# Optimization experiments

Hardware: AMD Instinct MI355X
Metric: run time of the kernel (lower is better)

## Reference

```python
import jax, jax.numpy as jnp
import numpy as np

B, T, C = 4, 2048, 1024
H = 16
D = C // H  # head_size = 64


def setup_inputs() -> dict:
    key = jax.random.key(0)
    k1, k2, k3 = jax.random.split(key, 3)
    x = jax.random.normal(k1, (B, T, C), dtype=jnp.float32)
    # weights stored pre-transposed relative to torch nn.Linear: y = x @ w
    w_attn = jax.random.normal(k2, (C, 3 * C), dtype=jnp.float32) * (1.0 / np.sqrt(C))
    w_proj = jax.random.normal(k3, (C, C), dtype=jnp.float32) * (1.0 / np.sqrt(C))
    return {"x": x, "w_attn": w_attn, "w_proj": w_proj}


def reference(x, w_attn, w_proj):
    # Dropout layers are identity in eval mode (reference baseline).
    Bx, Tx, Cx = x.shape
    qkv = x @ w_attn                                   # [B,T,3C]
    q, k, v = jnp.split(qkv, 3, axis=2)
    # [B,T,C] -> [B,H,T,D]
    def heads(t):
        return t.reshape(Bx, Tx, H, D).transpose(0, 2, 1, 3)
    q, k, v = heads(q), heads(k), heads(v)
    scale = 1.0 / np.sqrt(D).astype(np.float32)
    att = jnp.einsum('bhqd,bhkd->bhqk', q, k) * scale   # [B,H,T,T]
    causal = jnp.tril(jnp.ones((Tx, Tx), dtype=bool))
    att = jnp.where(causal[None, None], att, -jnp.inf)
    att = jax.nn.softmax(att, axis=-1)
    y = jnp.einsum('bhqk,bhkd->bhqd', att, v)           # [B,H,T,D]
    y = y.transpose(0, 2, 1, 3).reshape(Bx, Tx, Cx)     # [B,T,C]
    return y @ w_proj
```

## Files before the change

### kernel.cpp

```cpp
#include <hip/hip_runtime.h>

typedef unsigned short ushort;
typedef short short8 __attribute__((ext_vector_type(8)));
typedef short short4v __attribute__((ext_vector_type(4)));
typedef float f32x4 __attribute__((ext_vector_type(4)));
typedef __attribute__((address_space(3))) unsigned int lds_u32;
typedef __attribute__((address_space(1))) const unsigned int glb_u32;

#define DEVI static __device__ __forceinline__

DEVI ushort f2b(float f) {
  union { float f; unsigned u; } x; x.f = f;
  unsigned r = x.u + 0x7fffu + ((x.u >> 16) & 1u);
  return (ushort)(r >> 16);
}

DEVI void gload_lds16(const ushort* g, ushort* l) {
  __builtin_amdgcn_global_load_lds((glb_u32*)g, (lds_u32*)l, 16, 0, 0);
}

__global__ __launch_bounds__(256) void prep_kernel(
    const float* __restrict__ x, const float* __restrict__ wa,
    const float* __restrict__ wp, ushort* __restrict__ xb,
    ushort* __restrict__ watT, ushort* __restrict__ wpT) {
  __shared__ float tile[32][33];
  const int bid = blockIdx.x, tid = threadIdx.x;
  if (bid < 4096) {
    int i = bid * 256 + tid;
    const float4* p = (const float4*)x + 2 * (size_t)i;
    float4 a = p[0], b = p[1];
    ushort tmp[8] = { f2b(a.x), f2b(a.y), f2b(a.z), f2b(a.w),
                      f2b(b.x), f2b(b.y), f2b(b.z), f2b(b.w) };
    *(short8*)(xb + 8 * (size_t)i) = *(short8*)tmp;
    return;
  }
  const float* in; ushort* out; int R, C, bx, by;
  if (bid < 7168) {
    int bb = bid - 4096; in = wa; out = watT; R = 1024; C = 3072;
    bx = (bb % 96) * 32; by = (bb / 96) * 32;
  } else {
    int bb = bid - 7168; in = wp; out = wpT; R = 1024; C = 1024;
    bx = (bb % 32) * 32; by = (bb / 32) * 32;
  }
  const int tx = tid & 31, ty = tid >> 5;
#pragma unroll
  for (int i = 0; i < 32; i += 8)
    tile[ty + i][tx] = in[(size_t)(by + ty + i) * C + bx + tx];
  __syncthreads();
#pragma unroll
  for (int i = 0; i < 32; i += 8)
    out[(size_t)(bx + ty + i) * R + by + tx] = f2b(tile[tx][ty + i]);
}

template <bool OUT_F32, bool QKV>
__global__ __launch_bounds__(256) void gemm_bt_kernel(
    const ushort* __restrict__ A, const ushort* __restrict__ BT,
    void* __restrict__ C_, ushort* __restrict__ vt, int M, int N, int K) {
  __shared__ ushort lA[128 * 64];
  __shared__ ushort lB[128 * 64];
  const int tid = threadIdx.x, lane = tid & 63, wave = tid >> 6;
  const int wr = wave >> 1, wc = wave & 1;
  const int g = lane >> 4, c = lane & 15;
  const int m0 = blockIdx.x * 128, n0 = blockIdx.y * 128;

  const ushort* ap0; const ushort* ap1; const ushort* ap2; const ushort* ap3;
  const ushort* bp0; const ushort* bp1; const ushort* bp2; const ushort* bp3;
  {
    int r0 = tid >> 3,        c0 = (tid & 7) ^ (r0 & 7);
    int r1 = (256 + tid) >> 3, c1 = (tid & 7) ^ (r1 & 7);
    int r2 = (512 + tid) >> 3, c2 = (tid & 7) ^ (r2 & 7);
    int r3 = (768 + tid) >> 3, c3 = (tid & 7) ^ (r3 & 7);
    ap0 = A + (size_t)(m0 + r0) * K + c0 * 8;
    ap1 = A + (size_t)(m0 + r1) * K + c1 * 8;
    ap2 = A + (size_t)(m0 + r2) * K + c2 * 8;
    ap3 = A + (size_t)(m0 + r3) * K + c3 * 8;
    bp0 = BT + (size_t)(n0 + r0) * K + c0 * 8;
    bp1 = BT + (size_t)(n0 + r1) * K + c1 * 8;
    bp2 = BT + (size_t)(n0 + r2) * K + c2 * 8;
    bp3 = BT + (size_t)(n0 + r3) * K + c3 * 8;
  }

  f32x4 acc[4][4] = {};
  for (int kt = 0; kt < K; kt += 64) {
    __syncthreads();
    gload_lds16(ap0, lA + (size_t)tid * 8);
    gload_lds16(ap1, lA + (size_t)(256 + tid) * 8);
    gload_lds16(ap2, lA + (size_t)(512 + tid) * 8);
    gload_lds16(ap3, lA + (size_t)(768 + tid) * 8);
    gload_lds16(bp0, lB + (size_t)tid * 8);
    gload_lds16(bp1, lB + (size_t)(256 + tid) * 8);
    gload_lds16(bp2, lB + (size_t)(512 + tid) * 8);
    gload_lds16(bp3, lB + (size_t)(768 + tid) * 8);
    ap0 += 64; ap1 += 64; ap2 += 64; ap3 += 64;
    bp0 += 64; bp1 += 64; bp2 += 64; bp3 += 64;
    __syncthreads();
#pragma unroll
    for (int kk = 0; kk < 2; ++kk) {
      short8 af[4], bf[4];
#pragma unroll
      for (int mi = 0; mi < 4; ++mi) {
        int ra = wr * 64 + mi * 16 + c;
        af[mi] = *(const short8*)&lA[ra * 64 + (((kk * 4 + g) ^ (ra & 7)) * 8)];
      }
#pragma unroll
      for (int ni = 0; ni < 4; ++ni) {
        int rb = wc * 64 + ni * 16 + c;
        bf[ni] = *(const short8*)&lB[rb * 64 + (((kk * 4 + g) ^ (rb & 7)) * 8)];
      }
#pragma unroll
      for (int mi = 0; mi < 4; ++mi)
#pragma unroll
        for (int ni = 0; ni < 4; ++ni)
          acc[mi][ni] = __builtin_amdgcn_mfma_f32_16x16x32_bf16(af[mi], bf[ni], acc[mi][ni], 0, 0, 0);
    }
  }
  if (QKV && n0 >= 2048) {
#pragma unroll
    for (int mi = 0; mi < 4; ++mi)
#pragma unroll
      for (int ni = 0; ni < 4; ++ni) {
        int mrow0 = m0 + wr * 64 + mi * 16 + g * 4;
        int ncol = n0 - 2048 + wc * 64 + ni * 16 + c;
        int b = mrow0 >> 11, t0 = mrow0 & 2047;
        int hh = ncol >> 6, d = ncol & 63;
        ushort tmp[4] = { f2b(acc[mi][ni][0]), f2b(acc[mi][ni][1]),
                          f2b(acc[mi][ni][2]), f2b(acc[mi][ni][3]) };
        *(short4v*)&vt[((size_t)(b * 16 + hh) * 64 + d) * 2048 + t0] = *(short4v*)tmp;
      }
    return;
  }
#pragma unroll
  for (int mi = 0; mi < 4; ++mi)
#pragma unroll
    for (int ni = 0; ni < 4; ++ni)
#pragma unroll
      for (int r = 0; r < 4; ++r) {
        int mrow = m0 + wr * 64 + mi * 16 + g * 4 + r;
        int ncol = n0 + wc * 64 + ni * 16 + c;
        if (OUT_F32) ((float*)C_)[(size_t)mrow * N + ncol] = acc[mi][ni][r];
        else         ((ushort*)C_)[(size_t)mrow * N + ncol] = f2b(acc[mi][ni][r]);
      }
}

DEVI void attn_compute(const short8 (&qf)[2], f32x4 (&o)[4], float (&l)[4],
                       int qb_t, int kv, const ushort* __restrict__ kb,
                       const ushort* __restrict__ vb, ushort* __restrict__ pW,
                       int wave, int g, int c, int e) {
  const float C1 = 0.18033688011112042f;
  const float SH = 17.312340490667562f;
  f32x4 s[4];
#pragma unroll
  for (int n = 0; n < 4; ++n) {
    short8 kf0 = *(const short8*)&kb[(n * 16 + c) * 64 + ((g ^ e) * 8)];
    short8 kf1 = *(const short8*)&kb[(n * 16 + c) * 64 + (((4 + g) ^ e) * 8)];
    s[n] = (f32x4){0.f, 0.f, 0.f, 0.f};
    s[n] = __builtin_amdgcn_mfma_f32_16x16x32_bf16(qf[0], kf0, s[n], 0, 0, 0);
    s[n] = __builtin_amdgcn_mfma_f32_16x16x32_bf16(qf[1], kf1, s[n], 0, 0, 0);
  }
  if (kv == qb_t) {
#pragma unroll
    for (int n = 0; n < 4; ++n)
#pragma unroll
      for (int r = 0; r < 4; ++r)
        if ((n * 16 + c) > (wave * 16 + g * 4 + r)) s[n][r] = -INFINITY;
  }
#pragma unroll
  for (int n = 0; n < 4; ++n)
#pragma unroll
    for (int r = 0; r < 4; ++r) {
      float p = __builtin_amdgcn_exp2f(fmaf(s[n][r], C1, -SH));
      l[r] += p;
      union { float f; unsigned u; } pu; pu.f = p;
      int row = g * 4 + r;
      pW[row * 64 + (((n * 2 + (c >> 3)) ^ (row & 7)) * 8) + (c & 7)] =
          (ushort)((pu.u + 0x8000u) >> 16);
    }
  short8 pf0 = *(const short8*)&pW[c * 64 + ((g ^ e) * 8)];
  short8 pf1 = *(const short8*)&pW[c * 64 + (((4 + g) ^ e) * 8)];
#pragma unroll
  for (int dg = 0; dg < 4; ++dg) {
    short8 vf0 = *(const short8*)&vb[(dg * 16 + c) * 64 + ((g ^ e) * 8)];
    short8 vf1 = *(const short8*)&vb[(dg * 16 + c) * 64 + (((4 + g) ^ e) * 8)];
    o[dg] = __builtin_amdgcn_mfma_f32_16x16x32_bf16(pf0, vf0, o[dg], 0, 0, 0);
    o[dg] = __builtin_amdgcn_mfma_f32_16x16x32_bf16(pf1, vf1, o[dg], 0, 0, 0);
  }
}

DEVI void attn_store(const f32x4 (&o)[4], float (&l)[4], ushort* __restrict__ y,
                     int b, int h, int qb_t, int wave, int g, int c) {
#pragma unroll
  for (int r = 0; r < 4; ++r) {
    float s0 = l[r];
    s0 += __shfl_xor(s0, 1);
    s0 += __shfl_xor(s0, 2);
    s0 += __shfl_xor(s0, 4);
    s0 += __shfl_xor(s0, 8);
    l[r] = 1.0f / s0;
  }
#pragma unroll
  for (int dg = 0; dg < 4; ++dg)
#pragma unroll
    for (int r = 0; r < 4; ++r) {
      size_t row = (size_t)b * 2048 + qb_t * 64 + wave * 16 + g * 4 + r;
      y[row * 1024 + h * 64 + dg * 16 + c] = f2b(o[dg][r] * l[r]);
    }
}

__global__ __launch_bounds__(256, 2) void attn_kernel(
    const ushort* __restrict__ qkv, const ushort* __restrict__ vt,
    ushort* __restrict__ y) {
  __shared__ ushort kT[64 * 64];
  __shared__ ushort vT[64 * 64];
  __shared__ ushort pB[4][16 * 64];
  const int tid = threadIdx.x, lane = tid & 63, wave = tid >> 6;
  const int g = lane >> 4, c = lane & 15, e = c & 7;
  const int j = blockIdx.x, bh = blockIdx.y;
  const int b = bh >> 4, h = bh & 15;
  const int qb0 = j, qb1 = 31 - j;
  const size_t base = (size_t)b * 2048 * 3072 + (size_t)h * 64;
  const ushort* qp = qkv + base;
  const ushort* kp = qkv + base + 1024;
  const ushort* vp = vt + (size_t)bh * 64 * 2048;

  short8 qf0[2], qf1[2];
  {
    int qrow0 = qb0 * 64 + wave * 16 + c;
    int qrow1 = qb1 * 64 + wave * 16 + c;
    qf0[0] = *(const short8*)(qp + (size_t)qrow0 * 3072 + g * 8);
    qf0[1] = *(const short8*)(qp + (size_t)qrow0 * 3072 + 32 + g * 8);
    qf1[0] = *(const short8*)(qp + (size_t)qrow1 * 3072 + g * 8);
    qf1[1] = *(const short8*)(qp + (size_t)qrow1 * 3072 + 32 + g * 8);
  }
  f32x4 o0[4] = {}, o1[4] = {};
  float l0[4] = {0.f, 0.f, 0.f, 0.f}, l1[4] = {0.f, 0.f, 0.f, 0.f};

  short8 kr0, kr1, vr0, vr1;
  const int row0 = tid >> 3, ch0 = tid & 7;
  const int row1 = (256 + tid) >> 3, ch1 = tid & 7;
  const int cs0 = ch0 ^ (row0 & 7), cs1 = ch1 ^ (row1 & 7);

  auto issue = [&](int kv) {
    kr0 = *(const short8*)(kp + (size_t)(kv * 64 + row0) * 3072 + cs0 * 8);
    kr1 = *(const short8*)(kp + (size_t)(kv * 64 + row1) * 3072 + cs1 * 8);
    vr0 = *(const short8*)(vp + (size_t)row0 * 2048 + kv * 64 + cs0 * 8);
    vr1 = *(const short8*)(vp + (size_t)row1 * 2048 + kv * 64 + cs1 * 8);
  };
  auto commit = [&]() {
    *(short8*)&kT[tid * 8] = kr0;
    *(short8*)&kT[(256 + tid) * 8] = kr1;
    *(short8*)&vT[tid * 8] = vr0;
    *(short8*)&vT[(256 + tid) * 8] = vr1;
  };

  issue(0);
  for (int kv = 0; kv <= qb1; ++kv) {
    commit();
    __syncthreads();
    if (kv < qb1) issue(kv + 1);
    attn_compute(qf1, o1, l1, qb1, kv, kT, vT, pB[wave], wave, g, c, e);
    if (kv <= qb0)
      attn_compute(qf0, o0, l0, qb0, kv, kT, vT, pB[wave], wave, g, c, e);
    __syncthreads();
  }

  attn_store(o0, l0, y, b, h, qb0, wave, g, c);
  attn_store(o1, l1, y, b, h, qb1, wave, g, c);
}

extern "C" void kernel_launch(void* const* d_in, const int* in_sizes, int n_in,
                              void* d_out, int out_size, void* d_ws, size_t ws_size,
                              hipStream_t stream) {
  const float* x      = (const float*)d_in[0];
  const float* w_attn = (const float*)d_in[1];
  const float* w_proj = (const float*)d_in[2];
  float* out = (float*)d_out;

  ushort* xb   = (ushort*)d_ws;
  ushort* watT = xb   + (size_t)8192 * 1024;
  ushort* wpT  = watT + (size_t)3072 * 1024;
  ushort* qkvb = wpT  + (size_t)1024 * 1024;
  ushort* yb   = qkvb + (size_t)8192 * 3072;
  ushort* vtb  = yb   + (size_t)8192 * 1024;

  prep_kernel<<<8192, 256, 0, stream>>>(x, w_attn, w_proj, xb, watT, wpT);
  gemm_bt_kernel<false, true><<<dim3(64, 24), 256, 0, stream>>>(
      xb, watT, qkvb, vtb, 8192, 3072, 1024);
  attn_kernel<<<dim3(16, 64), 256, 0, stream>>>(qkvb, vtb, yb);
  gemm_bt_kernel<true, false><<<dim3(64, 8), 256, 0, stream>>>(
      yb, wpT, out, nullptr, 8192, 1024, 1024);
}
```

Before: 171.5 us.

## Split paired causal query blocks across 8 waves instead of serial per-wave

The attention block grows from 4 to 8 waves: waves 0-3 handle the late query block and waves 4-7 the early one, instead of each wave computing both blocks one after the other. Each thread now loads a single K/V chunk per tile, and register state per thread is halved, which allows higher occupancy. The early-block waves sit idle after their diagonal while the late-block waves keep iterating, so the work is unbalanced inside the block, and syncs now cover twice as many waves.

```diff
diff --git a/kernel.cpp b/kernel.cpp
--- a/kernel.cpp
+++ b/kernel.cpp
@@ -145,7 +145,7 @@
 DEVI void attn_compute(const short8 (&qf)[2], f32x4 (&o)[4], float (&l)[4],
                        int qb_t, int kv, const ushort* __restrict__ kb,
                        const ushort* __restrict__ vb, ushort* __restrict__ pW,
-                       int wave, int g, int c, int e) {
+                       int wrow, int g, int c, int e) {
   const float C1 = 0.18033688011112042f;
   const float SH = 17.312340490667562f;
   f32x4 s[4];
@@ -162,7 +162,7 @@
     for (int n = 0; n < 4; ++n)
 #pragma unroll
       for (int r = 0; r < 4; ++r)
-        if ((n * 16 + c) > (wave * 16 + g * 4 + r)) s[n][r] = -INFINITY;
+        if ((n * 16 + c) > (wrow * 16 + g * 4 + r)) s[n][r] = -INFINITY;
   }
 #pragma unroll
   for (int n = 0; n < 4; ++n)
@@ -187,7 +187,7 @@
 }
 
 DEVI void attn_store(const f32x4 (&o)[4], float (&l)[4], ushort* __restrict__ y,
-                     int b, int h, int qb_t, int wave, int g, int c) {
+                     int b, int h, int qb_t, int wrow, int g, int c) {
 #pragma unroll
   for (int r = 0; r < 4; ++r) {
     float s0 = l[r];
@@ -201,55 +201,49 @@
   for (int dg = 0; dg < 4; ++dg)
 #pragma unroll
     for (int r = 0; r < 4; ++r) {
-      size_t row = (size_t)b * 2048 + qb_t * 64 + wave * 16 + g * 4 + r;
+      size_t row = (size_t)b * 2048 + qb_t * 64 + wrow * 16 + g * 4 + r;
       y[row * 1024 + h * 64 + dg * 16 + c] = f2b(o[dg][r] * l[r]);
     }
 }
 
-__global__ __launch_bounds__(256, 2) void attn_kernel(
+__global__ __launch_bounds__(512, 4) void attn_kernel(
     const ushort* __restrict__ qkv, const ushort* __restrict__ vt,
     ushort* __restrict__ y) {
   __shared__ ushort kT[64 * 64];
   __shared__ ushort vT[64 * 64];
-  __shared__ ushort pB[4][16 * 64];
+  __shared__ ushort pB[8][16 * 64];
   const int tid = threadIdx.x, lane = tid & 63, wave = tid >> 6;
   const int g = lane >> 4, c = lane & 15, e = c & 7;
   const int j = blockIdx.x, bh = blockIdx.y;
   const int b = bh >> 4, h = bh & 15;
   const int qb0 = j, qb1 = 31 - j;
+  const int wrow = wave & 3;
+  const int myqb = (wave < 4) ? qb1 : qb0;
   const size_t base = (size_t)b * 2048 * 3072 + (size_t)h * 64;
   const ushort* qp = qkv + base;
   const ushort* kp = qkv + base + 1024;
   const ushort* vp = vt + (size_t)bh * 64 * 2048;
 
-  short8 qf0[2], qf1[2];
+  short8 qf[2];
   {
-    int qrow0 = qb0 * 64 + wave * 16 + c;
-    int qrow1 = qb1 * 64 + wave * 16 + c;
-    qf0[0] = *(const short8*)(qp + (size_t)qrow0 * 3072 + g * 8);
-    qf0[1] = *(const short8*)(qp + (size_t)qrow0 * 3072 + 32 + g * 8);
-    qf1[0] = *(const short8*)(qp + (size_t)qrow1 * 3072 + g * 8);
-    qf1[1] = *(const short8*)(qp + (size_t)qrow1 * 3072 + 32 + g * 8);
-  }
-  f32x4 o0[4] = {}, o1[4] = {};
-  float l0[4] = {0.f, 0.f, 0.f, 0.f}, l1[4] = {0.f, 0.f, 0.f, 0.f};
-
-  short8 kr0, kr1, vr0, vr1;
-  const int row0 = tid >> 3, ch0 = tid & 7;
-  const int row1 = (256 + tid) >> 3, ch1 = tid & 7;
-  const int cs0 = ch0 ^ (row0 & 7), cs1 = ch1 ^ (row1 & 7);
+    int qrow = myqb * 64 + wrow * 16 + c;
+    qf[0] = *(const short8*)(qp + (size_t)qrow * 3072 + g * 8);
+    qf[1] = *(const short8*)(qp + (size_t)qrow * 3072 + 32 + g * 8);
+  }
+  f32x4 o[4] = {};
+  float l[4] = {0.f, 0.f, 0.f, 0.f};
+
+  short8 kr, vr;
+  const int row = tid >> 3, ch = tid & 7;
+  const int cs = ch ^ (row & 7);
 
   auto issue = [&](int kv) {
-    kr0 = *(const short8*)(kp + (size_t)(kv * 64 + row0) * 3072 + cs0 * 8);
-    kr1 = *(const short8*)(kp + (size_t)(kv * 64 + row1) * 3072 + cs1 * 8);
-    vr0 = *(const short8*)(vp + (size_t)row0 * 2048 + kv * 64 + cs0 * 8);
-    vr1 = *(const short8*)(vp + (size_t)row1 * 2048 + kv * 64 + cs1 * 8);
+    kr = *(const short8*)(kp + (size_t)(kv * 64 + row) * 3072 + cs * 8);
+    vr = *(const short8*)(vp + (size_t)row * 2048 + kv * 64 + cs * 8);
   };
   auto commit = [&]() {
-    *(short8*)&kT[tid * 8] = kr0;
-    *(short8*)&kT[(256 + tid) * 8] = kr1;
-    *(short8*)&vT[tid * 8] = vr0;
-    *(short8*)&vT[(256 + tid) * 8] = vr1;
+    *(short8*)&kT[tid * 8] = kr;
+    *(short8*)&vT[tid * 8] = vr;
   };
 
   issue(0);
@@ -257,14 +251,12 @@
     commit();
     __syncthreads();
     if (kv < qb1) issue(kv + 1);
-    attn_compute(qf1, o1, l1, qb1, kv, kT, vT, pB[wave], wave, g, c, e);
-    if (kv <= qb0)
-      attn_compute(qf0, o0, l0, qb0, kv, kT, vT, pB[wave], wave, g, c, e);
-    __syncthreads();
-  }
-
-  attn_store(o0, l0, y, b, h, qb0, wave, g, c);
-  attn_store(o1, l1, y, b, h, qb1, wave, g, c);
+    if (kv <= myqb)
+      attn_compute(qf, o, l, myqb, kv, kT, vT, pB[wave], wrow, g, c, e);
+    __syncthreads();
+  }
+
+  attn_store(o, l, y, b, h, myqb, wrow, g, c);
 }
 
 extern "C" void kernel_launch(void* const* d_in, const int* in_sizes, int n_in,
@@ -285,7 +277,7 @@
   prep_kernel<<<8192, 256, 0, stream>>>(x, w_attn, w_proj, xb, watT, wpT);
   gemm_bt_kernel<false, true><<<dim3(64, 24), 256, 0, stream>>>(
       xb, watT, qkvb, vtb, 8192, 3072, 1024);
-  attn_kernel<<<dim3(16, 64), 256, 0, stream>>>(qkvb, vtb, yb);
+  attn_kernel<<<dim3(16, 64), 512, 0, stream>>>(qkvb, vtb, yb);
   gemm_bt_kernel<true, false><<<dim3(64, 8), 256, 0, stream>>>(
       yb, wpT, out, nullptr, 8192, 1024, 1024);
 }
```

Result: no change. 172.5 us (+0.6%).
